# Kernel tuning notes

Measured on AMD Instinct MI355X. Metric: run time of the kernel, lower is better.

The kernel has to match this reference:

```python
import jax, jax.numpy as jnp
import numpy as np

NEG = -1e4      # BigBird additive mask value
LN_EPS = 1e-12  # BERT-style LayerNorm eps


def _bigbird_forward(xs_pad, mask, Wq, bq, Wk, bk, Wv, bv, Wo, bo, gamma, beta, rand_idx):
    b, n, hsz = xs_pad.shape
    H = rand_idx.shape[0]
    nb = rand_idx.shape[1] + 2          # one rand row per non-edge query block
    BS = n // nb                        # block size
    d = hsz // H
    r = rand_idx.shape[2]
    scale = 1.0 / np.sqrt(d).astype(np.float32)

    mf = mask.reshape(b, n).astype(xs_pad.dtype)   # (b,n) 1=token, 0=pad
    mb = mf.reshape(b, nb, BS)                     # blocked mask

    def proj(W, bias):
        return (xs_pad @ W + bias).reshape(b, n, H, d).transpose(0, 2, 1, 3)

    q = proj(Wq, bq) * scale            # (b,H,n,d)
    k = proj(Wk, bk)
    v = proj(Wv, bv)
    qb = q.reshape(b, H, nb, BS, d)
    kb = k.reshape(b, H, nb, BS, d)
    vb = v.reshape(b, H, nb, BS, d)

    # ---- global rows: first / last query block attend to all keys ----
    def full_row(qi):                   # qi: (b,H,BS,d)
        s = jnp.einsum('bhqd,bhkd->bhqk', qi, k) + (1.0 - mf)[:, None, None, :] * NEG
        return jnp.einsum('bhqk,bhkd->bhqd', jax.nn.softmax(s, axis=-1), v)

    ctx_first = full_row(qb[:, :, 0])
    ctx_last = full_row(qb[:, :, nb - 1])

    # ---- random key/value blocks: per-head, per-query-block gather ----
    hidx = jnp.arange(H)[:, None, None]
    rand_k = kb[:, hidx, rand_idx].reshape(b, H, nb - 2, r * BS, d)
    rand_v = vb[:, hidx, rand_idx].reshape(b, H, nb - 2, r * BS, d)
    rand_m = mb[:, rand_idx].reshape(b, H, nb - 2, r * BS)

    def sparse_row(qi, kc, vc, mc):     # kc:(b,H,K,d), mc:(b,H,K)
        s = jnp.einsum('bhqd,bhkd->bhqk', qi, kc) + (1.0 - mc)[:, :, None, :] * NEG
        return jnp.einsum('bhqk,bhkd->bhqd', jax.nn.softmax(s, axis=-1), vc)

    def gather_blocks(ids, ridx):
        kc = jnp.concatenate([kb[:, :, j] for j in ids] + [rand_k[:, :, ridx]], axis=2)
        vc = jnp.concatenate([vb[:, :, j] for j in ids] + [rand_v[:, :, ridx]], axis=2)
        mc = jnp.concatenate([jnp.broadcast_to(mb[:, None, j], (b, H, BS)) for j in ids]
                             + [rand_m[:, :, ridx]], axis=2)
        return kc, vc, mc

    # second / penultimate query blocks: window + globals + rand
    ctx_second = sparse_row(qb[:, :, 1], *gather_blocks([0, 1, 2, nb - 1], 0))
    ctx_penult = sparse_row(qb[:, :, nb - 2], *gather_blocks([nb - 3, nb - 2, nb - 1, 0], nb - 3))

    # ---- middle rows i in [2, nb-3]: 3-block sliding window + first/last global + r random ----
    nmid = nb - 4
    mid = jnp.arange(2, nb - 2)
    win = mid[:, None] + jnp.arange(-1, 2)[None, :]        # (nmid,3)
    k_win = kb[:, :, win].reshape(b, H, nmid, 3 * BS, d)
    v_win = vb[:, :, win].reshape(b, H, nmid, 3 * BS, d)
    m_win = jnp.broadcast_to(mb[:, win].reshape(b, 1, nmid, 3 * BS), (b, H, nmid, 3 * BS))

    def rep_glob(t):                     # (b,H,BS,...) -> (b,H,nmid,BS,...)
        return jnp.broadcast_to(t[:, :, None], (b, H, nmid) + t.shape[2:])

    k_mid = jnp.concatenate([k_win, rep_glob(kb[:, :, 0]), rep_glob(kb[:, :, nb - 1]),
                             rand_k[:, :, 1:nb - 3]], axis=3)
    v_mid = jnp.concatenate([v_win, rep_glob(vb[:, :, 0]), rep_glob(vb[:, :, nb - 1]),
                             rand_v[:, :, 1:nb - 3]], axis=3)
    m_first = jnp.broadcast_to(mb[:, None, None, 0], (b, H, nmid, BS))
    m_last = jnp.broadcast_to(mb[:, None, None, nb - 1], (b, H, nmid, BS))
    m_mid = jnp.concatenate([m_win, m_first, m_last, rand_m[:, :, 1:nb - 3]], axis=3)

    s_mid = jnp.einsum('bhmqd,bhmkd->bhmqk', qb[:, :, 2:nb - 2], k_mid) \
            + (1.0 - m_mid)[:, :, :, None, :] * NEG
    ctx_mid = jnp.einsum('bhmqk,bhmkd->bhmqd', jax.nn.softmax(s_mid, axis=-1), v_mid)

    ctx = jnp.concatenate([ctx_first[:, :, None], ctx_second[:, :, None], ctx_mid,
                           ctx_penult[:, :, None], ctx_last[:, :, None]], axis=2)
    ctx = ctx.reshape(b, H, n, d).transpose(0, 2, 1, 3).reshape(b, n, hsz)
    ctx = ctx * mf[:, :, None]           # from_mask on output rows

    # BigBirdSelfOutput: dense + residual + LayerNorm (dropout=0 / eval)
    y = ctx @ Wo + bo + xs_pad
    mu = y.mean(-1, keepdims=True)
    var = ((y - mu) ** 2).mean(-1, keepdims=True)
    return (y - mu) * jax.lax.rsqrt(var + LN_EPS) * gamma + beta


def setup_inputs() -> dict:
    key = jax.random.key(0)
    ks = jax.random.split(key, 6)
    B, N, HSZ, H, BS, R = 4, 4096, 1024, 16, 64, 3
    NB = N // BS
    init = lambda k, shp: jax.random.normal(k, shp, dtype=jnp.float32) * 0.02
    return {
        'xs_pad': jax.random.normal(ks[0], (B, N, HSZ), dtype=jnp.float32),
        'mask': jnp.ones((B, 1, N), dtype=jnp.int32),
        'Wq': init(ks[1], (HSZ, HSZ)), 'bq': jnp.zeros((HSZ,), jnp.float32),
        'Wk': init(ks[2], (HSZ, HSZ)), 'bk': jnp.zeros((HSZ,), jnp.float32),
        'Wv': init(ks[3], (HSZ, HSZ)), 'bv': jnp.zeros((HSZ,), jnp.float32),
        'Wo': init(ks[4], (HSZ, HSZ)), 'bo': jnp.zeros((HSZ,), jnp.float32),
        'gamma': jnp.ones((HSZ,), jnp.float32), 'beta': jnp.zeros((HSZ,), jnp.float32),
        'rand_idx': jax.random.randint(ks[5], (H, NB - 2, R), 1, NB - 1).astype(jnp.int32),
    }


def reference(xs_pad, mask, Wq, bq, Wk, bk, Wv, bv, Wo, bo, gamma, beta, rand_idx):
    return _bigbird_forward(xs_pad, mask, Wq, bq, Wk, bk, Wv, bv, Wo, bo, gamma, beta, rand_idx)
```

## Files before the change

### kernel.cpp

```cpp
#include <hip/hip_runtime.h>
#include <hip/hip_bf16.h>

#define B_   4
#define N_   4096
#define HSZ  1024
#define H_   16
#define D_   64
#define NB_  64
#define R_   3
#define M_   (B_*N_)
#define NEGV (-1e4f)

typedef float f32x4 __attribute__((ext_vector_type(4)));
typedef short s16x8 __attribute__((ext_vector_type(8)));
typedef __bf16 b16x8 __attribute__((ext_vector_type(8)));

__device__ __forceinline__ f32x4 mfma16(s16x8 a, s16x8 b, f32x4 c) {
  return __builtin_amdgcn_mfma_f32_16x16x32_bf16(
      __builtin_bit_cast(b16x8, a), __builtin_bit_cast(b16x8, b), c, 0, 0, 0);
}

__device__ __forceinline__ short f2b(float x) {
  __hip_bfloat16 h = __float2bfloat16(x);
  return (short)__builtin_bit_cast(unsigned short, h);
}

__device__ __forceinline__ void gl_lds16(const short* g, short* l) {
  __builtin_amdgcn_global_load_lds(
      (const __attribute__((address_space(1))) unsigned int*)g,
      (__attribute__((address_space(3))) unsigned int*)l, 16, 0, 0);
}

__global__ __launch_bounds__(256) void k_conv(const float* __restrict__ in,
                                              short* __restrict__ out) {
  size_t i = ((size_t)blockIdx.x * 256 + threadIdx.x) * 8;
  float4 a = *(const float4*)&in[i];
  float4 b = *(const float4*)&in[i + 4];
  s16x8 o;
  o[0] = f2b(a.x); o[1] = f2b(a.y); o[2] = f2b(a.z); o[3] = f2b(a.w);
  o[4] = f2b(b.x); o[5] = f2b(b.y); o[6] = f2b(b.z); o[7] = f2b(b.w);
  *(s16x8*)&out[i] = o;
}

__global__ __launch_bounds__(256) void k_wt(const float* __restrict__ Wq,
                                            const float* __restrict__ Wk,
                                            const float* __restrict__ Wv,
                                            const float* __restrict__ Wo,
                                            short* __restrict__ out) {
  const int z = blockIdx.z;
  const float* src = (z == 0) ? Wq : (z == 1) ? Wk : (z == 2) ? Wv : Wo;
  short* dst = out + (size_t)z * HSZ * HSZ;
  __shared__ __align__(16) float t[64][68];
  const int tk = blockIdx.x * 64, tn = blockIdx.y * 64;
  const int tid = threadIdx.x;
#pragma unroll
  for (int r = 0; r < 4; ++r) {
    int c = tid + r * 256;
    int row = c >> 4, seg = c & 15;
    *(float4*)&t[row][seg * 4] =
        *(const float4*)&src[(size_t)(tk + row) * HSZ + tn + seg * 4];
  }
  __syncthreads();
#pragma unroll
  for (int r = 0; r < 2; ++r) {
    int c = tid + r * 256;
    int row = c >> 3, seg = c & 7;
    s16x8 o;
#pragma unroll
    for (int u = 0; u < 8; ++u) o[u] = f2b(t[seg * 8 + u][row]);
    *(s16x8*)&dst[(size_t)(tn + row) * HSZ + tk + seg * 8] = o;
  }
}

__global__ __launch_bounds__(256) void k_attb(const int* __restrict__ mask,
                                              float* __restrict__ attb) {
  int i = blockIdx.x * 256 + threadIdx.x;
  attb[i] = (1.0f - (float)mask[i]) * NEGV;
}

template <int MODE>
__global__ __launch_bounds__(256) void k_gemm(
    const short* __restrict__ A, const short* __restrict__ WT,
    const float* __restrict__ b0, const float* __restrict__ b1,
    const float* __restrict__ b2, short* __restrict__ o0,
    short* __restrict__ o1, short* __restrict__ o2,
    const float* __restrict__ xs, float* __restrict__ yout) {
  const int z = blockIdx.z;
  const short* Bt = WT + (size_t)z * HSZ * HSZ;
  const float* bias = (MODE == 0) ? ((z == 0) ? b0 : (z == 1) ? b1 : b2) : b0;
  short* outb = (z == 0) ? o0 : o1;
  const float alpha = (MODE == 0 && z == 0) ? 0.125f : 1.0f;

  __shared__ __align__(16) short lds_raw[17536];
  short (*a_lds)[64] = reinterpret_cast<short(*)[64]>(lds_raw);
  short (*b_lds)[64] = reinterpret_cast<short(*)[64]>(lds_raw + 8192);
  short (*t_lds)[137] = reinterpret_cast<short(*)[137]>(lds_raw);

  const int tid = threadIdx.x, lane = tid & 63, wave = tid >> 6;
  const int lq = lane & 15, g = lane >> 4;
  const int wm = (wave & 1) * 64, wn = (wave >> 1) * 64;
  const int tm = blockIdx.x * 128, tn = blockIdx.y * 128;

  const int srow = wave * 32 + (lane >> 3);
  const int scol = (lane & 7) * 8;

  f32x4 acc[4][4] = {};

  for (int kt = 0; kt < HSZ; kt += 64) {
    __syncthreads();
#pragma unroll
    for (int u = 0; u < 4; ++u) {
      gl_lds16(&A[(size_t)(tm + srow + u * 8) * HSZ + kt + scol],
               &a_lds[wave * 32 + u * 8][0]);
      gl_lds16(&Bt[(size_t)(tn + srow + u * 8) * HSZ + kt + scol],
               &b_lds[wave * 32 + u * 8][0]);
    }
    __syncthreads();
#pragma unroll
    for (int kk = 0; kk < 2; ++kk) {
      const int ko = kk * 32 + g * 8;
      s16x8 af[4], bf[4];
#pragma unroll
      for (int i = 0; i < 4; ++i)
        af[i] = *(const s16x8*)&a_lds[wm + i * 16 + lq][ko];
#pragma unroll
      for (int j = 0; j < 4; ++j)
        bf[j] = *(const s16x8*)&b_lds[wn + j * 16 + lq][ko];
#pragma unroll
      for (int i = 0; i < 4; ++i)
#pragma unroll
        for (int j = 0; j < 4; ++j)
          acc[i][j] = mfma16(af[i], bf[j], acc[i][j]);
    }
  }

  if (MODE == 0 && z == 2) {
    __syncthreads();
#pragma unroll
    for (int i = 0; i < 4; ++i)
#pragma unroll
      for (int j = 0; j < 4; ++j) {
        const int col_l = wn + j * 16 + lq;
        const float bi = bias[tn + col_l];
#pragma unroll
        for (int e = 0; e < 4; ++e) {
          const int row_l = wm + i * 16 + g * 4 + e;
          t_lds[col_l][row_l] = f2b(acc[i][j][e] + bi);
        }
      }
    __syncthreads();
    const int bb = tm >> 12;
    const int n0 = tm & (N_ - 1);
#pragma unroll
    for (int p = 0; p < 8; ++p) {
      int cc = tid + p * 256;
      int r = cc >> 4;
      int sg = cc & 15;
      int hh = (tn + r) >> 6, dd = (tn + r) & 63;
      *(s16x8*)&o2[(((size_t)bb * H_ + hh) * D_ + dd) * N_ + n0 + sg * 8] =
          *(const s16x8*)&t_lds[r][sg * 8];
    }
    return;
  }

#pragma unroll
  for (int i = 0; i < 4; ++i)
#pragma unroll
    for (int j = 0; j < 4; ++j) {
      const int col = tn + wn + j * 16 + lq;
#pragma unroll
      for (int e = 0; e < 4; ++e) {
        const int row = tm + wm + i * 16 + g * 4 + e;
        float v = acc[i][j][e];
        if (MODE == 0) {
          v = (v + bias[col]) * alpha;
          int bb = row >> 12, nn = row & (N_ - 1);
          int hh = col >> 6, dd = col & 63;
          outb[(((size_t)bb * H_ + hh) * N_ + nn) * D_ + dd] = f2b(v);
        } else {
          size_t idx = (size_t)row * HSZ + col;
          yout[idx] = v + bias[col] + xs[idx];
        }
      }
    }
}

__global__ __launch_bounds__(256) void k_attn(
    const short* __restrict__ Q, const short* __restrict__ K,
    const short* __restrict__ VT, const float* __restrict__ attb,
    const int* __restrict__ mask, const int* __restrict__ rnd,
    short* __restrict__ ctx, float* __restrict__ pO,
    float* __restrict__ pm, float* __restrict__ pl) {
  const int s = blockIdx.x, h = blockIdx.y, b = blockIdx.z;
  const int tid = threadIdx.x, lane = tid & 63, wave = tid >> 6;
  const int g = lane >> 4, lq = lane & 15;

  __shared__ __align__(16) short k_lds[64][72];
  __shared__ __align__(16) short vt_lds[64][72];
  __shared__ __align__(16) short p_lds[4][16][72];
  __shared__ __align__(16) float bias_s[64];
  __shared__ int list_s[8];
  __shared__ int Ls;

  const bool mid = (s < 62);
  const int qb = mid ? (s + 1) : (((s - 62) >> 3) ? (NB_ - 1) : 0);

  if (tid == 0) {
    int L;
    if (!mid) {
      int chunk = (s - 62) & 7;
#pragma unroll
      for (int i = 0; i < 8; ++i) list_s[i] = chunk * 8 + i;
      L = 8;
    } else {
      const int* rp = rnd + ((size_t)h * (NB_ - 2) + (qb - 1)) * R_;
      int n;
      if (qb == 1) {
        list_s[0] = 0; list_s[1] = 1; list_s[2] = 2; list_s[3] = NB_ - 1; n = 4;
      } else if (qb == NB_ - 2) {
        list_s[0] = NB_ - 3; list_s[1] = NB_ - 2; list_s[2] = NB_ - 1;
        list_s[3] = 0; n = 4;
      } else {
        list_s[0] = qb - 1; list_s[1] = qb; list_s[2] = qb + 1;
        list_s[3] = 0; list_s[4] = NB_ - 1; n = 5;
      }
      for (int j = 0; j < R_; ++j) list_s[n + j] = rp[j];
      L = n + R_;
    }
    Ls = L;
  }

  const size_t bh = (size_t)b * H_ + h;
  const size_t qrow = bh * N_ + (size_t)qb * 64 + wave * 16 + lq;
  s16x8 qf0 = *(const s16x8*)&Q[qrow * D_ + g * 8];
  s16x8 qf1 = *(const s16x8*)&Q[qrow * D_ + 32 + g * 8];

  __syncthreads();
  const int L = Ls;

  const int r0 = tid >> 3, sg0 = tid & 7;
  const int r1 = 32 + (tid >> 3), sg1 = tid & 7;

  s16x8 kr0, kr1, vr0, vr1;
  float br = 0.0f;
  {
    const int kb = list_s[0];
    const short* kp = &K[(bh * N_ + (size_t)kb * 64) * D_];
    const short* vp = &VT[bh * (size_t)D_ * N_ + (size_t)kb * 64];
    kr0 = *(const s16x8*)&kp[r0 * D_ + sg0 * 8];
    kr1 = *(const s16x8*)&kp[r1 * D_ + sg1 * 8];
    vr0 = *(const s16x8*)&vp[(size_t)r0 * N_ + sg0 * 8];
    vr1 = *(const s16x8*)&vp[(size_t)r1 * N_ + sg1 * 8];
    if (tid < 64) br = attb[(size_t)b * N_ + kb * 64 + tid];
  }

  f32x4 o[4] = {};
  float m_run = -INFINITY, ssum = 0.0f;

  for (int it = 0; it < L; ++it) {
    *(s16x8*)&k_lds[r0][sg0 * 8] = kr0;
    *(s16x8*)&k_lds[r1][sg1 * 8] = kr1;
    *(s16x8*)&vt_lds[r0][sg0 * 8] = vr0;
    *(s16x8*)&vt_lds[r1][sg1 * 8] = vr1;
    if (tid < 64) bias_s[tid] = br;
    if (it + 1 < L) {
      const int kb = list_s[it + 1];
      const short* kp = &K[(bh * N_ + (size_t)kb * 64) * D_];
      const short* vp = &VT[bh * (size_t)D_ * N_ + (size_t)kb * 64];
      kr0 = *(const s16x8*)&kp[r0 * D_ + sg0 * 8];
      kr1 = *(const s16x8*)&kp[r1 * D_ + sg1 * 8];
      vr0 = *(const s16x8*)&vp[(size_t)r0 * N_ + sg0 * 8];
      vr1 = *(const s16x8*)&vp[(size_t)r1 * N_ + sg1 * 8];
      if (tid < 64) br = attb[(size_t)b * N_ + kb * 64 + tid];
    }
    __syncthreads();

    f32x4 st[4];
#pragma unroll
    for (int f = 0; f < 4; ++f) {
      f32x4 acc0 = {};
#pragma unroll
      for (int kk = 0; kk < 2; ++kk) {
        s16x8 af = *(const s16x8*)&k_lds[f * 16 + lq][kk * 32 + g * 8];
        acc0 = mfma16(af, kk ? qf1 : qf0, acc0);
      }
      f32x4 b4 = *(const f32x4*)&bias_s[f * 16 + g * 4];
      st[f] = acc0 + b4;
    }

    float bm = -INFINITY;
#pragma unroll
    for (int f = 0; f < 4; ++f)
#pragma unroll
      for (int e = 0; e < 4; ++e) bm = fmaxf(bm, st[f][e]);
    bm = fmaxf(bm, __shfl_xor(bm, 16));
    bm = fmaxf(bm, __shfl_xor(bm, 32));
    float mnew = fmaxf(m_run, bm);
    float al = __expf(m_run - mnew);
    float psum = 0.0f;
#pragma unroll
    for (int f = 0; f < 4; ++f)
#pragma unroll
      for (int e = 0; e < 4; ++e) {
        float p = __expf(st[f][e] - mnew);
        st[f][e] = p;
        psum += p;
      }
    psum += __shfl_xor(psum, 16);
    psum += __shfl_xor(psum, 32);
    ssum = ssum * al + psum;
    m_run = mnew;

#pragma unroll
    for (int f = 0; f < 4; ++f) {
      unsigned int w0 = (unsigned short)f2b(st[f][0]) |
                        ((unsigned int)(unsigned short)f2b(st[f][1]) << 16);
      unsigned int w1 = (unsigned short)f2b(st[f][2]) |
                        ((unsigned int)(unsigned short)f2b(st[f][3]) << 16);
      *(uint2*)&p_lds[wave][lq][f * 16 + g * 4] = make_uint2(w0, w1);
    }

    float a0 = __shfl(al, g * 4 + 0);
    float a1 = __shfl(al, g * 4 + 1);
    float a2 = __shfl(al, g * 4 + 2);
    float a3 = __shfl(al, g * 4 + 3);
#pragma unroll
    for (int j = 0; j < 4; ++j) {
      o[j][0] *= a0; o[j][1] *= a1; o[j][2] *= a2; o[j][3] *= a3;
    }

#pragma unroll
    for (int kk = 0; kk < 2; ++kk) {
      s16x8 pa = *(const s16x8*)&p_lds[wave][lq][kk * 32 + g * 8];
#pragma unroll
      for (int j = 0; j < 4; ++j) {
        s16x8 bv = *(const s16x8*)&vt_lds[j * 16 + lq][kk * 32 + g * 8];
        o[j] = mfma16(pa, bv, o[j]);
      }
    }
    __syncthreads();
  }

  if (mid) {
    float rs = (float)mask[(size_t)b * N_ + qb * 64 + wave * 16 + lq] / ssum;
    float s0 = __shfl(rs, g * 4 + 0);
    float s1 = __shfl(rs, g * 4 + 1);
    float s2 = __shfl(rs, g * 4 + 2);
    float s3 = __shfl(rs, g * 4 + 3);
#pragma unroll
    for (int j = 0; j < 4; ++j) {
      k_lds[wave * 16 + g * 4 + 0][j * 16 + lq] = f2b(o[j][0] * s0);
      k_lds[wave * 16 + g * 4 + 1][j * 16 + lq] = f2b(o[j][1] * s1);
      k_lds[wave * 16 + g * 4 + 2][j * 16 + lq] = f2b(o[j][2] * s2);
      k_lds[wave * 16 + g * 4 + 3][j * 16 + lq] = f2b(o[j][3] * s3);
    }
    __syncthreads();
#pragma unroll
    for (int p = 0; p < 2; ++p) {
      int c = tid + p * 256;
      int row = c >> 3, seg = c & 7;
      *(s16x8*)&ctx[((size_t)b * N_ + qb * 64 + row) * HSZ + h * D_ + seg * 8] =
          *(const s16x8*)&k_lds[row][seg * 8];
    }
  } else {
    const int e2 = s - 62;
    const int qsel = e2 >> 3, chunk = e2 & 7;
    const size_t eidx = (bh * 2 + qsel) * 8 + chunk;
    float* po = pO + eidx * 4096;
#pragma unroll
    for (int j = 0; j < 4; ++j)
#pragma unroll
      for (int e = 0; e < 4; ++e)
        po[(wave * 16 + g * 4 + e) * 64 + j * 16 + lq] = o[j][e];
    if (lane < 16) {
      pm[eidx * 64 + wave * 16 + lane] = m_run;
      pl[eidx * 64 + wave * 16 + lane] = ssum;
    }
  }
}

__global__ __launch_bounds__(256) void k_comb(
    const float* __restrict__ pO, const float* __restrict__ pm,
    const float* __restrict__ pl, const int* __restrict__ mask,
    short* __restrict__ ctx) {
  const int qsel = blockIdx.x, h = blockIdx.y, b = blockIdx.z;
  const int qb = qsel ? NB_ - 1 : 0;
  const int tid = threadIdx.x;
  const int q = tid >> 2, dq = tid & 3;
  const size_t base = (((size_t)b * H_ + h) * 2 + qsel) * 8;

  float mv[8];
  float M = -INFINITY;
#pragma unroll
  for (int i = 0; i < 8; ++i) {
    mv[i] = pm[(base + i) * 64 + q];
    M = fmaxf(M, mv[i]);
  }
  float Lsum = 0.0f;
#pragma unroll
  for (int i = 0; i < 8; ++i) {
    float w = __expf(mv[i] - M);
    mv[i] = w;
    Lsum += pl[(base + i) * 64 + q] * w;
  }
  f32x4 acc[4] = {};
#pragma unroll
  for (int i = 0; i < 8; ++i) {
    const float* p = pO + (base + i) * 4096 + q * 64 + dq * 16;
    float w = mv[i];
#pragma unroll
    for (int u = 0; u < 4; ++u) {
      f32x4 v = *(const f32x4*)&p[u * 4];
      acc[u] += v * w;
    }
  }
  float sc = (float)mask[(size_t)b * N_ + qb * 64 + q] / Lsum;
  s16x8 out0, out1;
#pragma unroll
  for (int u = 0; u < 8; ++u) {
    out0[u] = f2b(acc[u >> 2][u & 3] * sc);
    out1[u] = f2b(acc[2 + (u >> 2)][u & 3] * sc);
  }
  short* dst = &ctx[((size_t)b * N_ + qb * 64 + q) * HSZ + h * D_ + dq * 16];
  *(s16x8*)dst = out0;
  *(s16x8*)(dst + 8) = out1;
}

__global__ __launch_bounds__(256) void k_ln(float* __restrict__ y,
                                            const float* __restrict__ gamma,
                                            const float* __restrict__ beta) {
  const int row = blockIdx.x, tid = threadIdx.x, lane = tid & 63,
            wave = tid >> 6;
  __shared__ float s_sum[4], s_sq[4];
  float4 v = *(const float4*)&y[(size_t)row * HSZ + tid * 4];
  float s = v.x + v.y + v.z + v.w;
  float q = v.x * v.x + v.y * v.y + v.z * v.z + v.w * v.w;
#pragma unroll
  for (int m = 1; m <= 32; m <<= 1) {
    s += __shfl_xor(s, m);
    q += __shfl_xor(q, m);
  }
  if (lane == 0) { s_sum[wave] = s; s_sq[wave] = q; }
  __syncthreads();
  float S = s_sum[0] + s_sum[1] + s_sum[2] + s_sum[3];
  float Qs = s_sq[0] + s_sq[1] + s_sq[2] + s_sq[3];
  float mu = S * (1.0f / HSZ);
  float var = Qs * (1.0f / HSZ) - mu * mu;
  float r = rsqrtf(var + 1e-12f);
  float4 g = *(const float4*)&gamma[tid * 4];
  float4 be = *(const float4*)&beta[tid * 4];
  float4 outv;
  outv.x = (v.x - mu) * r * g.x + be.x;
  outv.y = (v.y - mu) * r * g.y + be.y;
  outv.z = (v.z - mu) * r * g.z + be.z;
  outv.w = (v.w - mu) * r * g.w + be.w;
  *(float4*)&y[(size_t)row * HSZ + tid * 4] = outv;
}

extern "C" void kernel_launch(void* const* d_in, const int* in_sizes, int n_in,
                              void* d_out, int out_size, void* d_ws,
                              size_t ws_size, hipStream_t stream) {
  const float* xs = (const float*)d_in[0];
  const int* mask = (const int*)d_in[1];
  const float* Wq = (const float*)d_in[2];
  const float* bq = (const float*)d_in[3];
  const float* Wk = (const float*)d_in[4];
  const float* bk = (const float*)d_in[5];
  const float* Wv = (const float*)d_in[6];
  const float* bv = (const float*)d_in[7];
  const float* Wo = (const float*)d_in[8];
  const float* bo = (const float*)d_in[9];
  const float* gamma = (const float*)d_in[10];
  const float* beta = (const float*)d_in[11];
  const int* rnd = (const int*)d_in[12];
  float* yout = (float*)d_out;

  char* ws = (char*)d_ws;
  const size_t SZ_XS = (size_t)M_ * HSZ * 2;
  const size_t SZ_WT = (size_t)4 * HSZ * HSZ * 2;
  short* xsb = (short*)ws;
  short* wt = (short*)(ws + SZ_XS);
  short* qbuf = (short*)(ws + SZ_XS + SZ_WT);
  short* kbuf = qbuf + (size_t)M_ * HSZ;
  short* vtb = kbuf + (size_t)M_ * HSZ;
  char* after = ws + SZ_XS + SZ_WT + 3 * SZ_XS;
  float* attb = (float*)after;
  float* pO = (float*)(after + (1 << 20));
  float* pm = pO + (size_t)1024 * 4096;
  float* pl = pm + (size_t)1024 * 64;

  k_conv<<<8192, 256, 0, stream>>>(xs, xsb);
  k_wt<<<dim3(16, 16, 4), 256, 0, stream>>>(Wq, Wk, Wv, Wo, wt);
  k_attb<<<64, 256, 0, stream>>>(mask, attb);
  k_gemm<0><<<dim3(128, 8, 3), 256, 0, stream>>>(
      xsb, wt, bq, bk, bv, qbuf, kbuf, vtb, nullptr, nullptr);
  k_attn<<<dim3(78, H_, B_), 256, 0, stream>>>(qbuf, kbuf, vtb, attb, mask,
                                               rnd, xsb, pO, pm, pl);
  k_comb<<<dim3(2, H_, B_), 256, 0, stream>>>(pO, pm, pl, mask, xsb);
  k_gemm<1><<<dim3(128, 8, 1), 256, 0, stream>>>(
      xsb, wt + (size_t)3 * HSZ * HSZ, bo, nullptr, nullptr, nullptr, nullptr,
      nullptr, xs, yout);
  k_ln<<<M_, 256, 0, stream>>>(yout, gamma, beta);
}
```

Before: 399.8 us.

## Swizzle GEMM LDS tiles and vectorize epilogue stores via operand-swapped MFMA

The GEMM LDS tiles now use an XOR swizzle on the 16-byte column segment, so the fragment reads from LDS avoid bank conflicts. The MFMA operands are swapped for the Q/K and output projections, which puts four consecutive columns in each lane's accumulator. That lets bias, residual and bf16 stores be issued as float4 and uint2 vector accesses instead of scalar writes. The V projection becomes its own launch that writes the transposed V layout straight from registers, dropping the LDS transpose stage. This adds one kernel launch and relies on the swizzle matching the global_load_lds write pattern.

```diff
diff --git a/kernel.cpp b/kernel.cpp
--- a/kernel.cpp
+++ b/kernel.cpp
@@ -23,6 +23,11 @@
 __device__ __forceinline__ short f2b(float x) {
   __hip_bfloat16 h = __float2bfloat16(x);
   return (short)__builtin_bit_cast(unsigned short, h);
+}
+
+__device__ __forceinline__ unsigned pack2(float a, float b) {
+  return (unsigned)(unsigned short)f2b(a) |
+         ((unsigned)(unsigned short)f2b(b) << 16);
 }
 
 __device__ __forceinline__ void gl_lds16(const short* g, short* l) {
@@ -78,23 +83,21 @@
   attb[i] = (1.0f - (float)mask[i]) * NEGV;
 }
 
-template <int MODE>
+template <int PATH>
 __global__ __launch_bounds__(256) void k_gemm(
     const short* __restrict__ A, const short* __restrict__ WT,
-    const float* __restrict__ b0, const float* __restrict__ b1,
-    const float* __restrict__ b2, short* __restrict__ o0,
-    short* __restrict__ o1, short* __restrict__ o2,
+    const float* __restrict__ bias0, const float* __restrict__ bias1,
+    short* __restrict__ o0, short* __restrict__ o1,
     const float* __restrict__ xs, float* __restrict__ yout) {
-  const int z = blockIdx.z;
-  const short* Bt = WT + (size_t)z * HSZ * HSZ;
-  const float* bias = (MODE == 0) ? ((z == 0) ? b0 : (z == 1) ? b1 : b2) : b0;
-  short* outb = (z == 0) ? o0 : o1;
-  const float alpha = (MODE == 0 && z == 0) ? 0.125f : 1.0f;
-
-  __shared__ __align__(16) short lds_raw[17536];
-  short (*a_lds)[64] = reinterpret_cast<short(*)[64]>(lds_raw);
-  short (*b_lds)[64] = reinterpret_cast<short(*)[64]>(lds_raw + 8192);
-  short (*t_lds)[137] = reinterpret_cast<short(*)[137]>(lds_raw);
+  const int z = (PATH == 0) ? blockIdx.z : 0;
+  const int wsel = (PATH == 0) ? z : (PATH == 1 ? 2 : 3);
+  const short* Bt = WT + (size_t)wsel * HSZ * HSZ;
+  const float* bias = (PATH == 0 && z == 1) ? bias1 : bias0;
+  short* outb = (PATH == 0 && z == 1) ? o1 : o0;
+  const float alpha = (PATH == 0 && z == 0) ? 0.125f : 1.0f;
+
+  __shared__ __align__(16) short a_lds[128][64];
+  __shared__ __align__(16) short b_lds[128][64];
 
   const int tid = threadIdx.x, lane = tid & 63, wave = tid >> 6;
   const int lq = lane & 15, g = lane >> 4;
@@ -102,7 +105,7 @@
   const int tm = blockIdx.x * 128, tn = blockIdx.y * 128;
 
   const int srow = wave * 32 + (lane >> 3);
-  const int scol = (lane & 7) * 8;
+  const int scol = ((lane & 7) ^ ((lane >> 3) & 7)) * 8;
 
   f32x4 acc[4][4] = {};
 
@@ -116,9 +119,10 @@
                &b_lds[wave * 32 + u * 8][0]);
     }
     __syncthreads();
+    const int sw = (lq & 7) << 3;
 #pragma unroll
     for (int kk = 0; kk < 2; ++kk) {
-      const int ko = kk * 32 + g * 8;
+      const int ko = (kk * 32 + g * 8) ^ sw;
       s16x8 af[4], bf[4];
 #pragma unroll
       for (int i = 0; i < 4; ++i)
@@ -130,59 +134,58 @@
       for (int i = 0; i < 4; ++i)
 #pragma unroll
         for (int j = 0; j < 4; ++j)
-          acc[i][j] = mfma16(af[i], bf[j], acc[i][j]);
-    }
-  }
-
-  if (MODE == 0 && z == 2) {
-    __syncthreads();
-#pragma unroll
-    for (int i = 0; i < 4; ++i)
-#pragma unroll
-      for (int j = 0; j < 4; ++j) {
-        const int col_l = wn + j * 16 + lq;
-        const float bi = bias[tn + col_l];
-#pragma unroll
-        for (int e = 0; e < 4; ++e) {
-          const int row_l = wm + i * 16 + g * 4 + e;
-          t_lds[col_l][row_l] = f2b(acc[i][j][e] + bi);
-        }
-      }
-    __syncthreads();
-    const int bb = tm >> 12;
-    const int n0 = tm & (N_ - 1);
-#pragma unroll
-    for (int p = 0; p < 8; ++p) {
-      int cc = tid + p * 256;
-      int r = cc >> 4;
-      int sg = cc & 15;
-      int hh = (tn + r) >> 6, dd = (tn + r) & 63;
-      *(s16x8*)&o2[(((size_t)bb * H_ + hh) * D_ + dd) * N_ + n0 + sg * 8] =
-          *(const s16x8*)&t_lds[r][sg * 8];
-    }
-    return;
-  }
-
-#pragma unroll
-  for (int i = 0; i < 4; ++i)
+          acc[i][j] = (PATH == 1) ? mfma16(af[i], bf[j], acc[i][j])
+                                  : mfma16(bf[j], af[i], acc[i][j]);
+    }
+  }
+
+  if (PATH == 1) {
 #pragma unroll
     for (int j = 0; j < 4; ++j) {
       const int col = tn + wn + j * 16 + lq;
-#pragma unroll
-      for (int e = 0; e < 4; ++e) {
-        const int row = tm + wm + i * 16 + g * 4 + e;
-        float v = acc[i][j][e];
-        if (MODE == 0) {
-          v = (v + bias[col]) * alpha;
-          int bb = row >> 12, nn = row & (N_ - 1);
-          int hh = col >> 6, dd = col & 63;
-          outb[(((size_t)bb * H_ + hh) * N_ + nn) * D_ + dd] = f2b(v);
-        } else {
-          size_t idx = (size_t)row * HSZ + col;
-          yout[idx] = v + bias[col] + xs[idx];
-        }
+      const int hh = col >> 6, dd = col & 63;
+      const float bi = bias[col];
+#pragma unroll
+      for (int i = 0; i < 4; ++i) {
+        const int nrow = tm + wm + i * 16 + g * 4;
+        const int bb = nrow >> 12, nn = nrow & (N_ - 1);
+        uint2 w;
+        w.x = pack2(acc[i][j][0] + bi, acc[i][j][1] + bi);
+        w.y = pack2(acc[i][j][2] + bi, acc[i][j][3] + bi);
+        *(uint2*)&o0[(((size_t)bb * H_ + hh) * D_ + dd) * N_ + nn] = w;
       }
     }
+    return;
+  }
+
+#pragma unroll
+  for (int i = 0; i < 4; ++i) {
+    const int row = tm + wm + i * 16 + lq;
+#pragma unroll
+    for (int j = 0; j < 4; ++j) {
+      const int colb = tn + wn + j * 16 + g * 4;
+      const float4 bi = *(const float4*)&bias[colb];
+      if (PATH == 0) {
+        const int bb = row >> 12, nn = row & (N_ - 1);
+        const int hh = colb >> 6, dd = colb & 63;
+        uint2 w;
+        w.x = pack2((acc[i][j][0] + bi.x) * alpha,
+                    (acc[i][j][1] + bi.y) * alpha);
+        w.y = pack2((acc[i][j][2] + bi.z) * alpha,
+                    (acc[i][j][3] + bi.w) * alpha);
+        *(uint2*)&outb[(((size_t)bb * H_ + hh) * N_ + nn) * D_ + dd] = w;
+      } else {
+        const size_t idx = (size_t)row * HSZ + colb;
+        const float4 xv = *(const float4*)&xs[idx];
+        float4 yv;
+        yv.x = acc[i][j][0] + bi.x + xv.x;
+        yv.y = acc[i][j][1] + bi.y + xv.y;
+        yv.z = acc[i][j][2] + bi.z + xv.z;
+        yv.w = acc[i][j][3] + bi.w + xv.w;
+        *(float4*)&yout[idx] = yv;
+      }
+    }
+  }
 }
 
 __global__ __launch_bounds__(256) void k_attn(
@@ -313,11 +316,9 @@
 
 #pragma unroll
     for (int f = 0; f < 4; ++f) {
-      unsigned int w0 = (unsigned short)f2b(st[f][0]) |
-                        ((unsigned int)(unsigned short)f2b(st[f][1]) << 16);
-      unsigned int w1 = (unsigned short)f2b(st[f][2]) |
-                        ((unsigned int)(unsigned short)f2b(st[f][3]) << 16);
-      *(uint2*)&p_lds[wave][lq][f * 16 + g * 4] = make_uint2(w0, w1);
+      uint2 w = make_uint2(pack2(st[f][0], st[f][1]),
+                           pack2(st[f][2], st[f][3]));
+      *(uint2*)&p_lds[wave][lq][f * 16 + g * 4] = w;
     }
 
     float a0 = __shfl(al, g * 4 + 0);
@@ -492,13 +493,14 @@
   k_conv<<<8192, 256, 0, stream>>>(xs, xsb);
   k_wt<<<dim3(16, 16, 4), 256, 0, stream>>>(Wq, Wk, Wv, Wo, wt);
   k_attb<<<64, 256, 0, stream>>>(mask, attb);
-  k_gemm<0><<<dim3(128, 8, 3), 256, 0, stream>>>(
-      xsb, wt, bq, bk, bv, qbuf, kbuf, vtb, nullptr, nullptr);
+  k_gemm<0><<<dim3(128, 8, 2), 256, 0, stream>>>(
+      xsb, wt, bq, bk, qbuf, kbuf, nullptr, nullptr);
+  k_gemm<1><<<dim3(128, 8, 1), 256, 0, stream>>>(
+      xsb, wt, bv, nullptr, vtb, nullptr, nullptr, nullptr);
   k_attn<<<dim3(78, H_, B_), 256, 0, stream>>>(qbuf, kbuf, vtb, attb, mask,
                                                rnd, xsb, pO, pm, pl);
   k_comb<<<dim3(2, H_, B_), 256, 0, stream>>>(pO, pm, pl, mask, xsb);
-  k_gemm<1><<<dim3(128, 8, 1), 256, 0, stream>>>(
-      xsb, wt + (size_t)3 * HSZ * HSZ, bo, nullptr, nullptr, nullptr, nullptr,
-      nullptr, xs, yout);
+  k_gemm<2><<<dim3(128, 8, 1), 256, 0, stream>>>(
+      xsb, wt, bo, nullptr, nullptr, nullptr, xs, yout);
   k_ln<<<M_, 256, 0, stream>>>(yout, gamma, beta);
 }
```

Result: faster. 379.4 us (-5.1%).
